# Performance work log

Hardware: AMD Instinct MI355X
Metric: run time of the kernel (lower is better)

## Reference

```python
import jax, jax.numpy as jnp
import numpy as np

N_FREQS = 6  # PositionEmbedding N_freqs when embedding=='pe'

def _pe(x):
    freqs = (2.0 ** jnp.arange(N_FREQS)).astype(x.dtype)
    fx = x * freqs  # [B,Q,N_FREQS]
    sc = jnp.stack([jnp.sin(fx), jnp.cos(fx)], axis=-1).reshape(fx.shape[0], fx.shape[1], 2 * N_FREQS)
    return jnp.concatenate([x, sc], axis=-1)

def _mlp(h, W1, b1, W2, b2, W3, b3):
    h = jax.nn.relu(h @ W1 + b1)
    h = jax.nn.relu(h @ W2 + b2)
    return h @ W3 + b3

def setup_inputs() -> dict:
    key = jax.random.key(0)
    B, Q, N, D, H = 4, 65536, 8192, 16, 128
    ks = jax.random.split(key, 6)
    coord = jax.random.uniform(ks[0], (B, Q, 1), minval=-1.0, maxval=1.0, dtype=jnp.float32)
    latent = jax.random.normal(ks[1], (B, N, D), dtype=jnp.float32)
    in_dim = (1 + 2 * N_FREQS) + 3 * D  # pe(rel_coord) ++ unfolded feat = 13 + 48 = 61
    def init(k, shp, fan):
        return (jax.random.normal(k, shp, dtype=jnp.float32) / np.float32(np.sqrt(fan)))
    W1 = init(ks[2], (in_dim, H), in_dim); b1 = jnp.zeros((H,), jnp.float32)
    W2 = init(ks[3], (H, H), H);          b2 = jnp.zeros((H,), jnp.float32)
    W3 = init(ks[4], (H, 1), H);          b3 = jnp.zeros((1,), jnp.float32)
    return dict(coord=coord, latent=latent, W1=W1, b1=b1, W2=W2, b2=b2, W3=W3, b3=b3)

def reference(coord, latent, W1, b1, W2, b2, W3, b3):
    B, Q, _ = coord.shape
    N = latent.shape[1]
    # feat_unfold: concat shifted-prev / self / shifted-next along feature dim -> [B,N,3D]
    prev = jnp.concatenate([latent[:, :1], latent[:, :-1]], axis=1)
    nxt = jnp.concatenate([latent[:, 1:], latent[:, -1:]], axis=1)
    feat = jnp.concatenate([prev, latent, nxt], axis=-1)
    # make_coord grid: cell centers in [-1,1]
    grid = (-1.0 + (2.0 * jnp.arange(N, dtype=coord.dtype) + 1.0) / N)
    rx = 1.0 / N           # 2/num_latents/2
    eps_shift = 1e-6
    preds, areas = [], []
    for vx in (-2.0, 0.0):  # eval path vx_lst
        c = jnp.clip(coord + vx * rx + eps_shift, -1.0 + 1e-6, 1.0 - 1e-6)
        idx = jnp.clip(jnp.searchsorted(grid, c[..., 0]), 0, N - 1)  # [B,Q]
        q_coord = grid[idx][..., None]                               # [B,Q,1]
        q_feat = jnp.take_along_axis(feat, idx[..., None], axis=1)   # [B,Q,3D]
        rel = (coord - q_coord) * N                                  # scaled rel coord
        area = jnp.abs(rel[..., 0]) + 1e-9                           # [B,Q]
        inp = jnp.concatenate([_pe(rel), q_feat], axis=-1)           # [B,Q,61]
        preds.append(_mlp(inp, W1, b1, W2, b2, W3, b3))              # [B,Q,1]
        areas.append(area)
    tot = areas[0] + areas[1]
    # local_ensemble: swap areas before weighting
    ret = preds[0] * (areas[1] / tot)[..., None] + preds[1] * (areas[0] / tot)[..., None]
    return ret
```

## Files before the change

kernel.cpp:

```cpp
#include <hip/hip_runtime.h>
#include <hip/hip_bf16.h>

typedef short s8v __attribute__((ext_vector_type(8)));
typedef float f4v __attribute__((ext_vector_type(4)));
typedef unsigned u4v __attribute__((ext_vector_type(4)));

__device__ __forceinline__ unsigned short f2bf(float x) {
  unsigned u = __builtin_bit_cast(unsigned, x);
  u += 0x7fffu + ((u >> 16) & 1u);
  return (unsigned short)(u >> 16);
}
#if __has_builtin(__builtin_amdgcn_cvt_pk_bf16_f32)
__device__ __forceinline__ unsigned pk2(float a, float b) {
  return __builtin_bit_cast(unsigned, __builtin_amdgcn_cvt_pk_bf16_f32(a, b));
}
#else
__device__ __forceinline__ unsigned pk2(float a, float b) {
  unsigned ua = __builtin_bit_cast(unsigned, a) + 0x8000u;
  unsigned ub = __builtin_bit_cast(unsigned, b) + 0x8000u;
  return __builtin_amdgcn_perm(ub, ua, 0x07060302u);
}
#endif

__device__ __forceinline__ void g2lds16(const void* g, void* l) {
  __builtin_amdgcn_global_load_lds(
      (const __attribute__((address_space(1))) unsigned*)g,
      (__attribute__((address_space(3))) unsigned*)l, 16, 0, 0);
}

__global__ void prep_kernel(const float* __restrict__ W1, const float* __restrict__ b1,
                            const float* __restrict__ W2, const float* __restrict__ latent,
                            unsigned short* __restrict__ wsW) {
  int e = blockIdx.x * 256 + threadIdx.x;
  if (e < 8192) {
    int frag = e >> 9, rem = e & 511, lane = rem >> 3, j = rem & 7;
    int h = frag >> 1, ks = frag & 1;
    int q4 = lane >> 4, l15 = lane & 15;
    int k = ks * 32 + q4 * 8 + j;
    int n = h * 16 + l15;
    float v;
    if (k < 13) v = W1[k * 128 + n];
    else if (k == 13) v = b1[n];
    else if (k < 16) v = 0.0f;
    else v = W1[(k - 3) * 128 + n];
    wsW[e] = f2bf(v);
  } else if (e < 24576) {
    int e2 = e - 8192;
    int frag = e2 >> 9, rem = e2 & 511, lane = rem >> 3, j = rem & 7;
    int h2 = frag >> 2, ks = frag & 3;
    int q4 = lane >> 4, l15 = lane & 15;
    int kd = (j < 4) ? (32 * ks + 4 * q4 + j) : (32 * ks + 16 + 4 * q4 + (j - 4));
    int n = h2 * 16 + l15;
    wsW[e] = f2bf(W2[kd * 128 + n]);
  } else {
    int i = e - 24576;
    float4 v = ((const float4*)latent)[i];
    uint2 o;
    o.x = pk2(v.x, v.y);
    o.y = pk2(v.z, v.w);
    ((uint2*)(wsW + 24576))[i] = o;
  }
}

__global__ __launch_bounds__(256, 2) void lisagon_main(
    const float* __restrict__ coord, const unsigned short* __restrict__ latbf,
    const unsigned short* __restrict__ W1f, const unsigned short* __restrict__ W2f,
    const float* __restrict__ b2, const float* __restrict__ W3,
    const float* __restrict__ b3, float* __restrict__ out) {
  __shared__ __align__(16) unsigned short W2s[16384];
  __shared__ __align__(16) unsigned PE[2][256][4];
  __shared__ __align__(16) float BW[256];

  const int t = threadIdx.x;
  const int lane = t & 63, wv = t >> 6;
  const int l15 = lane & 15, q4 = lane >> 4;

  const int Rg = blockIdx.x * 256 + t;
  const int gq = Rg >> 1, p = Rg & 1;
  const float co = coord[gq];

  const s8v* W1fv = (const s8v*)W1f;
  s8v W1r[16];
#pragma unroll
  for (int i = 0; i < 16; i++) W1r[i] = W1fv[i * 64 + lane];

  int idx;
  float area;
  {
    float c = (co + (p ? 0.0f : -0.000244140625f)) + 1e-6f;
    c = fminf(fmaxf(c, -1.0f + 1e-6f), 1.0f - 1e-6f);
    double u = ((double)c * 8192.0 + 8191.0) * 0.5;
    idx = (int)ceil(u);
    idx = min(max(idx, 0), 8191);
    float qc = ((float)(2 * idx + 1) - 8192.0f) * (1.0f / 8192.0f);
    float rel = (co - qc) * 8192.0f;
    area = fabsf(rel) + 1e-9f;
    float v[16];
    v[0] = rel;
    float f = rel;
#pragma unroll
    for (int i = 0; i < 6; i++) {
      v[1 + 2 * i] = __sinf(f);
      v[2 + 2 * i] = __cosf(f);
      f = f + f;
    }
    v[13] = 1.0f;
    v[14] = 0.0f; v[15] = 0.0f;
    uint4 q0, q1;
    q0.x = pk2(v[0], v[1]);   q0.y = pk2(v[2], v[3]);
    q0.z = pk2(v[4], v[5]);   q0.w = pk2(v[6], v[7]);
    q1.x = pk2(v[8], v[9]);   q1.y = pk2(v[10], v[11]);
    q1.z = pk2(v[12], v[13]); q1.w = pk2(v[14], v[15]);
    ((uint4*)PE[0])[t] = q0;
    ((uint4*)PE[1])[t] = q1;
  }

  const size_t bbase = (size_t)(blockIdx.x >> 9) * (8192 * 16);
  const uint4* latv4 = (const uint4*)(latbf + bbase);
  const int rbase = wv * 64;
  const int c = q4 & 1;
  uint4 g0[4], g1[4];
#pragma unroll
  for (int rt = 0; rt < 4; rt++) {
    int srcl = rt * 16 + l15;
    int sidx = __shfl(idx, srcl, 64);
    int rp = max(sidx - 1, 0), rn = min(sidx + 1, 8191);
    g0[rt] = latv4[rp * 2 + c];
    g1[rt] = latv4[(q4 < 2 ? sidx : rn) * 2 + c];
  }

#pragma unroll
  for (int it = 0; it < 8; it++) {
    int off = (it * 4 + wv) * 1024;
    g2lds16((const char*)W2f + off + lane * 16, (char*)W2s + off);
  }
  if (t < 64) {
    ((float4*)BW)[t] = (t < 32) ? ((const float4*)b2)[t] : ((const float4*)W3)[t - 32];
  }

  s8v Bf[2][4];
#pragma unroll
  for (int rt = 0; rt < 4; rt++) {
    int srcl = rt * 16 + l15;
    uint4 pe = ((const uint4*)PE[c])[rbase + srcl];
    uint4 b0;
    b0.x = q4 < 2 ? pe.x : g0[rt].x;  b0.y = q4 < 2 ? pe.y : g0[rt].y;
    b0.z = q4 < 2 ? pe.z : g0[rt].z;  b0.w = q4 < 2 ? pe.w : g0[rt].w;
    Bf[0][rt] = __builtin_bit_cast(s8v, b0);
    Bf[1][rt] = __builtin_bit_cast(s8v, g1[rt]);
  }

  u4v bbv[4][4];
#pragma unroll
  for (int h = 0; h < 8; h++) {
    f4v a[4];
#pragma unroll
    for (int rt = 0; rt < 4; rt++) a[rt] = (f4v){0.f, 0.f, 0.f, 0.f};
#pragma unroll
    for (int ks = 0; ks < 2; ks++) {
#pragma unroll
      for (int rt = 0; rt < 4; rt++)
        a[rt] = __builtin_amdgcn_mfma_f32_16x16x32_bf16(W1r[h * 2 + ks], Bf[ks][rt],
                                                        a[rt], 0, 0, 0);
    }
#pragma unroll
    for (int rt = 0; rt < 4; rt++) {
      bbv[rt][h >> 1][2 * (h & 1)]     = pk2(fmaxf(a[rt][0], 0.f), fmaxf(a[rt][1], 0.f));
      bbv[rt][h >> 1][2 * (h & 1) + 1] = pk2(fmaxf(a[rt][2], 0.f), fmaxf(a[rt][3], 0.f));
    }
  }

  __syncthreads();

  const s8v* W2sv = (const s8v*)W2s;
  float s[4] = {0.f, 0.f, 0.f, 0.f};
#pragma unroll
  for (int h2 = 0; h2 < 8; h2++) {
    f4v a2[4];
    f4v b2v = ((const f4v*)BW)[h2 * 4 + q4];
#pragma unroll
    for (int rt = 0; rt < 4; rt++) a2[rt] = b2v;
#pragma unroll
    for (int ks = 0; ks < 4; ks++) {
      s8v Af = W2sv[(h2 * 4 + ks) * 64 + lane];
#pragma unroll
      for (int rt = 0; rt < 4; rt++)
        a2[rt] = __builtin_amdgcn_mfma_f32_16x16x32_bf16(
            Af, __builtin_bit_cast(s8v, bbv[rt][ks]), a2[rt], 0, 0, 0);
    }
    float4 w3v = ((const float4*)(BW + 128))[h2 * 4 + q4];
#pragma unroll
    for (int rt = 0; rt < 4; rt++) {
      s[rt] += fmaxf(a2[rt][0], 0.f) * w3v.x;
      s[rt] += fmaxf(a2[rt][1], 0.f) * w3v.y;
      s[rt] += fmaxf(a2[rt][2], 0.f) * w3v.z;
      s[rt] += fmaxf(a2[rt][3], 0.f) * w3v.w;
    }
  }

  const float b3s = b3[0];
#pragma unroll
  for (int rt = 0; rt < 4; rt++) {
    float pred = s[rt];
    pred += __shfl_xor(pred, 16, 64);
    pred += __shfl_xor(pred, 32, 64);
    pred += b3s;
    float other = __shfl_xor(pred, 1, 64);
    float a0 = __shfl(area, rt * 16 + l15, 64);
    float a1 = __shfl(area, rt * 16 + l15 + 1, 64);
    if (q4 == 0 && (l15 & 1) == 0) {
      int row0 = rbase + rt * 16 + l15;
      float tot = a0 + a1;
      out[(blockIdx.x * 256 + row0) >> 1] = pred * (a1 / tot) + other * (a0 / tot);
    }
  }
}

extern "C" void kernel_launch(void* const* d_in, const int* in_sizes, int n_in,
                              void* d_out, int out_size, void* d_ws, size_t ws_size,
                              hipStream_t stream) {
  const float* coord  = (const float*)d_in[0];
  const float* latent = (const float*)d_in[1];
  const float* W1 = (const float*)d_in[2];
  const float* b1 = (const float*)d_in[3];
  const float* W2 = (const float*)d_in[4];
  const float* b2 = (const float*)d_in[5];
  const float* W3 = (const float*)d_in[6];
  const float* b3 = (const float*)d_in[7];
  float* out = (float*)d_out;
  unsigned short* wsW = (unsigned short*)d_ws;

  prep_kernel<<<608, 256, 0, stream>>>(W1, b1, W2, latent, wsW);
  lisagon_main<<<2048, 256, 0, stream>>>(coord, wsW + 24576, wsW, wsW + 8192,
                                         b2, W3, b3, out);
}
```

Measured before the change: 96.98 us.

## Split row tiles into two halves, stream W1 from global, prefetch second gather

Processes the four row tiles per wave in two passes of two tiles, reducing accumulator and activation register footprint. W1 fragments are now loaded from global inside the GEMM1 loop instead of being held in 16 registers, and b2/W3 are read from global rather than staged in LDS. The latent gather for the second half is issued before the first half's GEMM2 so its latency overlaps with compute. This trades more W1/W2 fragment reloads and extra instruction overhead for lower register pressure and overlap.

```diff
diff --git a/kernel.cpp b/kernel.cpp
--- a/kernel.cpp
+++ b/kernel.cpp
@@ -69,27 +69,22 @@
     const float* __restrict__ b3, float* __restrict__ out) {
   __shared__ __align__(16) unsigned short W2s[16384];
   __shared__ __align__(16) unsigned PE[2][256][4];
-  __shared__ __align__(16) float BW[256];
 
   const int t = threadIdx.x;
   const int lane = t & 63, wv = t >> 6;
   const int l15 = lane & 15, q4 = lane >> 4;
+  const int c = q4 & 1;
 
   const int Rg = blockIdx.x * 256 + t;
   const int gq = Rg >> 1, p = Rg & 1;
   const float co = coord[gq];
 
-  const s8v* W1fv = (const s8v*)W1f;
-  s8v W1r[16];
-#pragma unroll
-  for (int i = 0; i < 16; i++) W1r[i] = W1fv[i * 64 + lane];
-
   int idx;
   float area;
   {
-    float c = (co + (p ? 0.0f : -0.000244140625f)) + 1e-6f;
-    c = fminf(fmaxf(c, -1.0f + 1e-6f), 1.0f - 1e-6f);
-    double u = ((double)c * 8192.0 + 8191.0) * 0.5;
+    float cc = (co + (p ? 0.0f : -0.000244140625f)) + 1e-6f;
+    cc = fminf(fmaxf(cc, -1.0f + 1e-6f), 1.0f - 1e-6f);
+    double u = ((double)cc * 8192.0 + 8191.0) * 0.5;
     idx = (int)ceil(u);
     idx = min(max(idx, 0), 8191);
     float qc = ((float)(2 * idx + 1) - 8192.0f) * (1.0f / 8192.0f);
@@ -118,102 +113,115 @@
   const size_t bbase = (size_t)(blockIdx.x >> 9) * (8192 * 16);
   const uint4* latv4 = (const uint4*)(latbf + bbase);
   const int rbase = wv * 64;
-  const int c = q4 & 1;
-  uint4 g0[4], g1[4];
-#pragma unroll
-  for (int rt = 0; rt < 4; rt++) {
+  const s8v* W1fv = (const s8v*)W1f;
+  const s8v* W2sv = (const s8v*)W2s;
+
+  uint4 G0[2], G1[2];
+  auto gather = [&](int rt, int r) {
     int srcl = rt * 16 + l15;
     int sidx = __shfl(idx, srcl, 64);
     int rp = max(sidx - 1, 0), rn = min(sidx + 1, 8191);
-    g0[rt] = latv4[rp * 2 + c];
-    g1[rt] = latv4[(q4 < 2 ? sidx : rn) * 2 + c];
-  }
+    G0[r] = latv4[rp * 2 + c];
+    G1[r] = latv4[(q4 < 2 ? sidx : rn) * 2 + c];
+  };
+
+  gather(0, 0);
+  gather(1, 1);
 
 #pragma unroll
   for (int it = 0; it < 8; it++) {
     int off = (it * 4 + wv) * 1024;
     g2lds16((const char*)W2f + off + lane * 16, (char*)W2s + off);
   }
-  if (t < 64) {
-    ((float4*)BW)[t] = (t < 32) ? ((const float4*)b2)[t] : ((const float4*)W3)[t - 32];
-  }
-
-  s8v Bf[2][4];
-#pragma unroll
-  for (int rt = 0; rt < 4; rt++) {
+
+  s8v Bfp[2][2];
+  auto bf_sel = [&](int rt, int r) {
     int srcl = rt * 16 + l15;
     uint4 pe = ((const uint4*)PE[c])[rbase + srcl];
     uint4 b0;
-    b0.x = q4 < 2 ? pe.x : g0[rt].x;  b0.y = q4 < 2 ? pe.y : g0[rt].y;
-    b0.z = q4 < 2 ? pe.z : g0[rt].z;  b0.w = q4 < 2 ? pe.w : g0[rt].w;
-    Bf[0][rt] = __builtin_bit_cast(s8v, b0);
-    Bf[1][rt] = __builtin_bit_cast(s8v, g1[rt]);
-  }
-
-  u4v bbv[4][4];
-#pragma unroll
-  for (int h = 0; h < 8; h++) {
-    f4v a[4];
-#pragma unroll
-    for (int rt = 0; rt < 4; rt++) a[rt] = (f4v){0.f, 0.f, 0.f, 0.f};
-#pragma unroll
-    for (int ks = 0; ks < 2; ks++) {
-#pragma unroll
-      for (int rt = 0; rt < 4; rt++)
-        a[rt] = __builtin_amdgcn_mfma_f32_16x16x32_bf16(W1r[h * 2 + ks], Bf[ks][rt],
-                                                        a[rt], 0, 0, 0);
-    }
-#pragma unroll
-    for (int rt = 0; rt < 4; rt++) {
-      bbv[rt][h >> 1][2 * (h & 1)]     = pk2(fmaxf(a[rt][0], 0.f), fmaxf(a[rt][1], 0.f));
-      bbv[rt][h >> 1][2 * (h & 1) + 1] = pk2(fmaxf(a[rt][2], 0.f), fmaxf(a[rt][3], 0.f));
-    }
-  }
-
+    b0.x = q4 < 2 ? pe.x : G0[r].x;  b0.y = q4 < 2 ? pe.y : G0[r].y;
+    b0.z = q4 < 2 ? pe.z : G0[r].z;  b0.w = q4 < 2 ? pe.w : G0[r].w;
+    Bfp[0][r] = __builtin_bit_cast(s8v, b0);
+    Bfp[1][r] = __builtin_bit_cast(s8v, G1[r]);
+  };
+
+  u4v bbv[2][4];
+  auto do_gemm1 = [&]() {
+#pragma unroll
+    for (int h = 0; h < 8; h++) {
+      f4v a[2];
+      a[0] = (f4v){0.f, 0.f, 0.f, 0.f};
+      a[1] = (f4v){0.f, 0.f, 0.f, 0.f};
+#pragma unroll
+      for (int ks = 0; ks < 2; ks++) {
+        s8v Af = W1fv[(h * 2 + ks) * 64 + lane];
+#pragma unroll
+        for (int r = 0; r < 2; r++)
+          a[r] = __builtin_amdgcn_mfma_f32_16x16x32_bf16(Af, Bfp[ks][r], a[r], 0, 0, 0);
+      }
+#pragma unroll
+      for (int r = 0; r < 2; r++) {
+        bbv[r][h >> 1][2 * (h & 1)]     = pk2(fmaxf(a[r][0], 0.f), fmaxf(a[r][1], 0.f));
+        bbv[r][h >> 1][2 * (h & 1) + 1] = pk2(fmaxf(a[r][2], 0.f), fmaxf(a[r][3], 0.f));
+      }
+    }
+  };
+
+  const float b3s = b3[0];
+  auto do_gemm2_epi = [&](int rt0) {
+    float s[2] = {0.f, 0.f};
+#pragma unroll
+    for (int h2 = 0; h2 < 8; h2++) {
+      f4v b2v = ((const f4v*)b2)[h2 * 4 + q4];
+      f4v a2[2];
+      a2[0] = b2v; a2[1] = b2v;
+#pragma unroll
+      for (int ks = 0; ks < 4; ks++) {
+        s8v Af = W2sv[(h2 * 4 + ks) * 64 + lane];
+#pragma unroll
+        for (int r = 0; r < 2; r++)
+          a2[r] = __builtin_amdgcn_mfma_f32_16x16x32_bf16(
+              Af, __builtin_bit_cast(s8v, bbv[r][ks]), a2[r], 0, 0, 0);
+      }
+      float4 w3v = ((const float4*)W3)[h2 * 4 + q4];
+#pragma unroll
+      for (int r = 0; r < 2; r++) {
+        s[r] += fmaxf(a2[r][0], 0.f) * w3v.x;
+        s[r] += fmaxf(a2[r][1], 0.f) * w3v.y;
+        s[r] += fmaxf(a2[r][2], 0.f) * w3v.z;
+        s[r] += fmaxf(a2[r][3], 0.f) * w3v.w;
+      }
+    }
+#pragma unroll
+    for (int r = 0; r < 2; r++) {
+      float pred = s[r];
+      pred += __shfl_xor(pred, 16, 64);
+      pred += __shfl_xor(pred, 32, 64);
+      pred += b3s;
+      float other = __shfl_xor(pred, 1, 64);
+      int rt = rt0 + r;
+      float a0 = __shfl(area, rt * 16 + l15, 64);
+      float a1 = __shfl(area, rt * 16 + l15 + 1, 64);
+      if (q4 == 0 && (l15 & 1) == 0) {
+        int row0 = rbase + rt * 16 + l15;
+        float tot = a0 + a1;
+        out[(blockIdx.x * 256 + row0) >> 1] = pred * (a1 / tot) + other * (a0 / tot);
+      }
+    }
+  };
+
+  bf_sel(0, 0);
+  bf_sel(1, 1);
+  do_gemm1();
   __syncthreads();
-
-  const s8v* W2sv = (const s8v*)W2s;
-  float s[4] = {0.f, 0.f, 0.f, 0.f};
-#pragma unroll
-  for (int h2 = 0; h2 < 8; h2++) {
-    f4v a2[4];
-    f4v b2v = ((const f4v*)BW)[h2 * 4 + q4];
-#pragma unroll
-    for (int rt = 0; rt < 4; rt++) a2[rt] = b2v;
-#pragma unroll
-    for (int ks = 0; ks < 4; ks++) {
-      s8v Af = W2sv[(h2 * 4 + ks) * 64 + lane];
-#pragma unroll
-      for (int rt = 0; rt < 4; rt++)
-        a2[rt] = __builtin_amdgcn_mfma_f32_16x16x32_bf16(
-            Af, __builtin_bit_cast(s8v, bbv[rt][ks]), a2[rt], 0, 0, 0);
-    }
-    float4 w3v = ((const float4*)(BW + 128))[h2 * 4 + q4];
-#pragma unroll
-    for (int rt = 0; rt < 4; rt++) {
-      s[rt] += fmaxf(a2[rt][0], 0.f) * w3v.x;
-      s[rt] += fmaxf(a2[rt][1], 0.f) * w3v.y;
-      s[rt] += fmaxf(a2[rt][2], 0.f) * w3v.z;
-      s[rt] += fmaxf(a2[rt][3], 0.f) * w3v.w;
-    }
-  }
-
-  const float b3s = b3[0];
-#pragma unroll
-  for (int rt = 0; rt < 4; rt++) {
-    float pred = s[rt];
-    pred += __shfl_xor(pred, 16, 64);
-    pred += __shfl_xor(pred, 32, 64);
-    pred += b3s;
-    float other = __shfl_xor(pred, 1, 64);
-    float a0 = __shfl(area, rt * 16 + l15, 64);
-    float a1 = __shfl(area, rt * 16 + l15 + 1, 64);
-    if (q4 == 0 && (l15 & 1) == 0) {
-      int row0 = rbase + rt * 16 + l15;
-      float tot = a0 + a1;
-      out[(blockIdx.x * 256 + row0) >> 1] = pred * (a1 / tot) + other * (a0 / tot);
-    }
-  }
+  gather(2, 0);
+  gather(3, 1);
+  do_gemm2_epi(0);
+
+  bf_sel(2, 0);
+  bf_sel(3, 1);
+  do_gemm1();
+  do_gemm2_epi(2);
 }
 
 extern "C" void kernel_launch(void* const* d_in, const int* in_sizes, int n_in,
```

Result: no change. 98.76 us (+1.8%).
